# Performance work log

Measured on AMD Instinct MI355X. Metric: run time of the kernel, lower is better.

Reference implementation:

```python
import jax, jax.numpy as jnp
import numpy as np

M = 512          # feature_dim
NH = 8           # num_heads
FFN = 2048       # ffn_hidden_dim
NMOD = 4         # modalities (seq len for attention)
EPS = 1e-5


def setup_inputs() -> dict:
    key = jax.random.key(0)
    ks = jax.random.split(key, 16)
    B, H = 64, 256
    s = 0.02
    return {
        "x_image": jax.random.normal(ks[0], (B, H, M), jnp.float32),
        "x_radar": jax.random.normal(ks[1], (B, H, M), jnp.float32),
        "x_lidar": jax.random.normal(ks[2], (B, H, M), jnp.float32),
        "x_gps":   jax.random.normal(ks[3], (B, H, M), jnp.float32),
        # nn.MultiheadAttention params (torch layout: weight is (out,in))
        "in_proj_w": jax.random.normal(ks[4], (3 * M, M), jnp.float32) * s,
        "in_proj_b": jnp.zeros((3 * M,), jnp.float32),
        "out_proj_w": jax.random.normal(ks[5], (M, M), jnp.float32) * s,
        "out_proj_b": jnp.zeros((M,), jnp.float32),
        "ln1_g": jnp.ones((M,), jnp.float32),
        "ln1_b": jnp.zeros((M,), jnp.float32),
        "w1": jax.random.normal(ks[6], (FFN, M), jnp.float32) * s,
        "b1": jnp.zeros((FFN,), jnp.float32),
        "w2": jax.random.normal(ks[7], (M, FFN), jnp.float32) * s,
        "b2": jnp.zeros((M,), jnp.float32),
        "ln2_g": jnp.ones((M,), jnp.float32),
        "ln2_b": jnpp if False else jnp.zeros((M,), jnp.float32),
    }


def _layernorm(x, g, b):
    mu = jnp.mean(x, axis=-1, keepdims=True)
    var = jnp.mean((x - mu) ** 2, axis=-1, keepdims=True)
    return (x - mu) * jax.lax.rsqrt(var + EPS) * g + b


def _forward(x_image, x_radar, x_lidar, x_gps,
             in_proj_w, in_proj_b, out_proj_w, out_proj_b,
             ln1_g, ln1_b, w1, b1, w2, b2, ln2_g, ln2_b):
    B, H, _ = x_image.shape
    # F: (B*H, NMOD, M) -- fold batch and time; per-t loop is independent
    F = jnp.stack([x_image, x_radar, x_lidar, x_gps], axis=2).reshape(B * H, NMOD, M)
    qkv = F @ in_proj_w.T + in_proj_b              # (N, NMOD, 3M)
    q, k, v = jnp.split(qkv, 3, axis=-1)
    dh = M // NH
    def heads(t):  # (N, NMOD, M) -> (N, NH, NMOD, dh)
        return t.reshape(-1, NMOD, NH, dh).transpose(0, 2, 1, 3)
    qh, kh, vh = heads(q), heads(k), heads(v)
    scores = jnp.einsum("bhsd,bhtd->bhst", qh, kh) / np.sqrt(dh).astype(np.float32)
    attn = jax.nn.softmax(scores, axis=-1)
    o = jnp.einsum("bhst,bhtd->bhsd", attn, vh)
    o = o.transpose(0, 2, 1, 3).reshape(-1, NMOD, M)
    attn_out = o @ out_proj_w.T + out_proj_b
    h1 = _layernorm(F + attn_out, ln1_g, ln1_b)    # (N, NMOD, M)
    agg = h1.sum(axis=1)                            # (N, M)
    ffn = jax.nn.gelu(agg @ w1.T + b1, approximate=False) @ w2.T + b2
    z = _layernorm(agg + ffn, ln2_g, ln2_b)
    return z.reshape(B, H, M)


def reference(x_image, x_radar, x_lidar, x_gps,
              in_proj_w, in_proj_b, out_proj_w, out_proj_b,
              ln1_g, ln1_b, w1, b1, w2, b2, ln2_g, ln2_b):
    return _forward(x_image, x_radar, x_lidar, x_gps,
                    in_proj_w, in_proj_b, out_proj_w, out_proj_b,
                    ln1_g, ln1_b, w1, b1, w2, b2, ln2_g, ln2_b)
```

## Files before the change

kernel.cpp:

```cpp
#include <hip/hip_runtime.h>
#include <hip/hip_bf16.h>


typedef __attribute__((ext_vector_type(8))) short s16x8;
typedef __attribute__((ext_vector_type(4))) float f32x4;

__device__ __forceinline__ unsigned short f2bf(float f) {
  unsigned int u = __float_as_uint(f);
  u += 0x7fffu + ((u >> 16) & 1u);
  return (unsigned short)(u >> 16);
}
__device__ __forceinline__ float bf2f(unsigned short s) {
  return __uint_as_float(((unsigned int)s) << 16);
}
__device__ __forceinline__ f32x4 mfma16(s16x8 a, s16x8 b, f32x4 c) {
  return __builtin_amdgcn_mfma_f32_16x16x32_bf16(a, b, c, 0, 0, 0);
}
__device__ __forceinline__ int swz(int row, int bir) {
  return row * 128 + ((((row) & 7) << 4) ^ bir);
}
__device__ __forceinline__ int vtoff(int r, int c) {
  return r * 1024 + ((c * 2) ^ ((r & 7) << 4));
}

__global__ void pack_kernel(const float* __restrict__ wqkv, const float* __restrict__ wout,
                            const float* __restrict__ w1, const float* __restrict__ w2,
                            const float* __restrict__ x0, const float* __restrict__ x1,
                            const float* __restrict__ x2, const float* __restrict__ x3,
                            unsigned short* __restrict__ o_wqkv, unsigned short* __restrict__ o_wout,
                            unsigned short* __restrict__ o_w1, unsigned short* __restrict__ o_w2,
                            unsigned short* __restrict__ o_x4) {
  const long c0 = 196608, c1 = 262144, c2 = 524288, c3 = 786432, c4 = 9175040;
  for (long v = (long)blockIdx.x * blockDim.x + threadIdx.x; v < c4;
       v += (long)gridDim.x * blockDim.x) {
    const float* src;
    unsigned short* dst;
    if (v < c0) { src = wqkv + v * 4; dst = o_wqkv + v * 4; }
    else if (v < c1) { long u = v - c0; src = wout + u * 4; dst = o_wout + u * 4; }
    else if (v < c2) { long u = v - c1; src = w1 + u * 4; dst = o_w1 + u * 4; }
    else if (v < c3) { long u = v - c2; src = w2 + u * 4; dst = o_w2 + u * 4; }
    else {
      long u = v - c3; long e = u * 4; long r = e >> 9; int i = (int)(e & 511);
      int s = (int)(r & 3); long n = r >> 2;
      const float* xs = (s == 0) ? x0 : (s == 1) ? x1 : (s == 2) ? x2 : x3;
      src = xs + n * 512 + i; dst = o_x4 + e;
    }
    float4 f = *reinterpret_cast<const float4*>(src);
    ushort4 hb;
    hb.x = f2bf(f.x); hb.y = f2bf(f.y); hb.z = f2bf(f.z); hb.w = f2bf(f.w);
    *reinterpret_cast<ushort4*>(dst) = hb;
  }
}

__launch_bounds__(256)
__global__ void qkv_attn_kernel(const unsigned short* __restrict__ x4,
                                const unsigned short* __restrict__ wqkv,
                                const float* __restrict__ in_b,
                                unsigned short* __restrict__ o_out) {
  const int wg = blockIdx.x;
  const int slot = wg >> 3, xcd = wg & 7;
  const int tb = ((slot >> 3) << 3) | xcd;
  const int h = slot & 7;
  const int tid = threadIdx.x, lane = tid & 63, w = tid >> 6;
  const int wm = w >> 1, wn = w & 1;
  const int QS = 200;

  __shared__ __align__(16) unsigned char smem[53248];
  unsigned short* aT = (unsigned short*)smem;
  unsigned short* bT = (unsigned short*)(smem + 16384);
  unsigned short* qkvT = (unsigned short*)smem;
  float* scoresLds = (float*)(smem + 51200);

  f32x4 acc[4][6];
#pragma unroll
  for (int i = 0; i < 4; ++i)
#pragma unroll
    for (int j = 0; j < 6; ++j) acc[i][j] = (f32x4){0.f, 0.f, 0.f, 0.f};

  const long rowBase = (long)tb * 128;

  for (int kk = 0; kk < 8; ++kk) {
    const int k0 = kk * 64;
#pragma unroll
    for (int it = 0; it < 4; ++it) {
      int cid = tid + it * 256, lr = cid >> 3, c8 = cid & 7;
      s16x8 v = *(const s16x8*)(x4 + (rowBase + lr) * 512 + k0 + c8 * 8);
      *(s16x8*)((unsigned char*)aT + swz(lr, c8 * 16)) = v;
    }
#pragma unroll
    for (int it = 0; it < 6; ++it) {
      int cid = tid + it * 256, bc = cid >> 3, c8 = cid & 7;
      int wrow = (bc < 64) ? (h * 64 + bc)
                : (bc < 128) ? (512 + h * 64 + (bc - 64))
                             : (1024 + h * 64 + (bc - 128));
      s16x8 v = *(const s16x8*)(wqkv + (long)wrow * 512 + k0 + c8 * 8);
      *(s16x8*)((unsigned char*)bT + swz(bc, c8 * 16)) = v;
    }
    __syncthreads();
#pragma unroll
    for (int k2 = 0; k2 < 2; ++k2) {
      s16x8 af[4], bfr[6];
      const int bir = k2 * 64 + ((lane >> 4) << 4);
#pragma unroll
      for (int mi = 0; mi < 4; ++mi) {
        int row = wm * 64 + mi * 16 + (lane & 15);
        af[mi] = *(const s16x8*)((unsigned char*)aT + swz(row, bir));
      }
#pragma unroll
      for (int ni = 0; ni < 6; ++ni) {
        int col = wn * 96 + ni * 16 + (lane & 15);
        bfr[ni] = *(const s16x8*)((unsigned char*)bT + swz(col, bir));
      }
#pragma unroll
      for (int mi = 0; mi < 4; ++mi)
#pragma unroll
        for (int ni = 0; ni < 6; ++ni)
          acc[mi][ni] = mfma16(af[mi], bfr[ni], acc[mi][ni]);
    }
    __syncthreads();
  }

#pragma unroll
  for (int mi = 0; mi < 4; ++mi)
#pragma unroll
    for (int ni = 0; ni < 6; ++ni) {
      int col = wn * 96 + ni * 16 + (lane & 15);
      int wrow = (col < 64) ? (h * 64 + col)
                : (col < 128) ? (512 + h * 64 + (col - 64))
                              : (1024 + h * 64 + (col - 128));
      float bias = in_b[wrow];
      int row0 = wm * 64 + mi * 16 + ((lane >> 4) << 2);
#pragma unroll
      for (int r = 0; r < 4; ++r)
        qkvT[(row0 + r) * QS + col] = f2bf(acc[mi][ni][r] + bias);
    }
  __syncthreads();

  const int token = tid >> 3, sub = tid & 7;
  {
    int p0 = sub * 2;
#pragma unroll
    for (int pp = 0; pp < 2; ++pp) {
      int p = p0 + pp, s = p >> 2, t = p & 3;
      const unsigned short* qr = qkvT + (token * 4 + s) * QS;
      const unsigned short* kr = qkvT + (token * 4 + t) * QS + 64;
      float d = 0.f;
#pragma unroll
      for (int c = 0; c < 8; ++c) {
        s16x8 qv = *(const s16x8*)(qr + c * 8);
        s16x8 kv = *(const s16x8*)(kr + c * 8);
#pragma unroll
        for (int i = 0; i < 8; ++i)
          d += bf2f((unsigned short)qv[i]) * bf2f((unsigned short)kv[i]);
      }
      scoresLds[token * 16 + p] = d * 0.125f;
    }
  }
  __syncthreads();
  float attnP[4][4];
#pragma unroll
  for (int s = 0; s < 4; ++s) {
    float m = -1e30f;
#pragma unroll
    for (int t = 0; t < 4; ++t) m = fmaxf(m, scoresLds[token * 16 + s * 4 + t]);
    float sum = 0.f;
#pragma unroll
    for (int t = 0; t < 4; ++t) {
      float e = expf(scoresLds[token * 16 + s * 4 + t] - m);
      attnP[s][t] = e; sum += e;
    }
    float inv = 1.f / sum;
#pragma unroll
    for (int t = 0; t < 4; ++t) attnP[s][t] *= inv;
  }
  float vv[4][8];
#pragma unroll
  for (int t = 0; t < 4; ++t) {
    s16x8 vvec = *(const s16x8*)(qkvT + (token * 4 + t) * QS + 128 + sub * 8);
#pragma unroll
    for (int d = 0; d < 8; ++d) vv[t][d] = bf2f((unsigned short)vvec[d]);
  }
#pragma unroll
  for (int s = 0; s < 4; ++s) {
    long orow = rowBase + token * 4 + s;
    unsigned short* dst = o_out + orow * 512 + h * 64 + sub * 8;
    s16x8 ov;
#pragma unroll
    for (int d = 0; d < 8; ++d) {
      float o = 0.f;
#pragma unroll
      for (int t = 0; t < 4; ++t) o += attnP[s][t] * vv[t][d];
      ov[d] = (short)f2bf(o);
    }
    *(s16x8*)dst = ov;
  }
}

__launch_bounds__(256)
__global__ void outproj_ln1_kernel(const unsigned short* __restrict__ o_in,
                                   const unsigned short* __restrict__ wout,
                                   const float* __restrict__ out_b,
                                   const float* __restrict__ x0, const float* __restrict__ x1,
                                   const float* __restrict__ x2, const float* __restrict__ x3,
                                   const float* __restrict__ ln1_g, const float* __restrict__ ln1_b,
                                   float* __restrict__ agg_f, unsigned short* __restrict__ agg_b) {
  const int tb = blockIdx.x;
  const int tid = threadIdx.x, lane = tid & 63, w = tid >> 6;
  __shared__ __align__(16) unsigned char smem[53504];
  unsigned short* vt = (unsigned short*)smem;
  unsigned short* aT = (unsigned short*)(smem + 32768);
  unsigned short* bT = (unsigned short*)(smem + 36864);
  float* stats = (float*)(smem + 53248);
  const long rowBase = (long)tb * 32;
  const float* xs[4] = {x0, x1, x2, x3};

  for (int ns = 0; ns < 4; ++ns) {
    f32x4 acc[2][2];
#pragma unroll
    for (int i = 0; i < 2; ++i)
#pragma unroll
      for (int j = 0; j < 2; ++j) acc[i][j] = (f32x4){0.f, 0.f, 0.f, 0.f};
    for (int kk = 0; kk < 8; ++kk) {
      const int k0 = kk * 64;
      {
        int lr = tid >> 3, c8 = tid & 7;
        s16x8 v = *(const s16x8*)(o_in + (rowBase + lr) * 512 + k0 + c8 * 8);
        *(s16x8*)((unsigned char*)aT + swz(lr, c8 * 16)) = v;
      }
#pragma unroll
      for (int it = 0; it < 4; ++it) {
        int cid = tid + it * 256, bc = cid >> 3, c8 = cid & 7;
        s16x8 v = *(const s16x8*)(wout + (long)(ns * 128 + bc) * 512 + k0 + c8 * 8);
        *(s16x8*)((unsigned char*)bT + swz(bc, c8 * 16)) = v;
      }
      __syncthreads();
#pragma unroll
      for (int k2 = 0; k2 < 2; ++k2) {
        s16x8 af[2], bfr[2];
        const int bir = k2 * 64 + ((lane >> 4) << 4);
#pragma unroll
        for (int mi = 0; mi < 2; ++mi) {
          int row = mi * 16 + (lane & 15);
          af[mi] = *(const s16x8*)((unsigned char*)aT + swz(row, bir));
        }
#pragma unroll
        for (int ni = 0; ni < 2; ++ni) {
          int col = w * 32 + ni * 16 + (lane & 15);
          bfr[ni] = *(const s16x8*)((unsigned char*)bT + swz(col, bir));
        }
#pragma unroll
        for (int mi = 0; mi < 2; ++mi)
#pragma unroll
          for (int ni = 0; ni < 2; ++ni)
            acc[mi][ni] = mfma16(af[mi], bfr[ni], acc[mi][ni]);
      }
      __syncthreads();
    }
#pragma unroll
    for (int mi = 0; mi < 2; ++mi)
#pragma unroll
      for (int ni = 0; ni < 2; ++ni) {
        int gcol = ns * 128 + w * 32 + ni * 16 + (lane & 15);
        float bias = out_b[gcol];
        int row0 = mi * 16 + ((lane >> 4) << 2);
#pragma unroll
        for (int r = 0; r < 4; ++r) {
          int rr = row0 + r;
          long grow = rowBase + rr;
          int s = (int)(grow & 3); long n = grow >> 2;
          float F = xs[s][n * 512 + gcol];
          *(unsigned short*)((unsigned char*)vt + vtoff(rr, gcol)) =
              f2bf(acc[mi][ni][r] + bias + F);
        }
      }
  }
  __syncthreads();
  {
    int wv = tid >> 6, ln = tid & 63;
    for (int i = 0; i < 8; ++i) {
      int r = wv * 8 + i;
      s16x8 v8 = *(const s16x8*)((unsigned char*)vt + vtoff(r, ln * 8));
      float sum = 0.f, sq = 0.f;
#pragma unroll
      for (int d = 0; d < 8; ++d) {
        float v = bf2f((unsigned short)v8[d]);
        sum += v; sq += v * v;
      }
#pragma unroll
      for (int off = 1; off < 64; off <<= 1) {
        sum += __shfl_xor(sum, off); sq += __shfl_xor(sq, off);
      }
      if (ln == 0) {
        float mu = sum * (1.f / 512.f);
        float var = sq * (1.f / 512.f) - mu * mu;
        stats[r * 2] = mu;
        stats[r * 2 + 1] = rsqrtf(var + 1e-5f);
      }
    }
  }
  __syncthreads();
  for (int it = 0; it < 2; ++it) {
    int ci = tid + it * 256;
    int tok = ci >> 6, c0 = (ci & 63) * 8;
    long gtok = (long)tb * 8 + tok;
    float a[8] = {0.f, 0.f, 0.f, 0.f, 0.f, 0.f, 0.f, 0.f};
#pragma unroll
    for (int s = 0; s < 4; ++s) {
      int r = tok * 4 + s;
      s16x8 v8 = *(const s16x8*)((unsigned char*)vt + vtoff(r, c0));
      float mu = stats[r * 2], is = stats[r * 2 + 1];
#pragma unroll
      for (int d = 0; d < 8; ++d) a[d] += (bf2f((unsigned short)v8[d]) - mu) * is;
    }
    float4 g0 = *(const float4*)(ln1_g + c0);
    float4 g1 = *(const float4*)(ln1_g + c0 + 4);
    float4 b0 = *(const float4*)(ln1_b + c0);
    float4 b1 = *(const float4*)(ln1_b + c0 + 4);
    float ov[8];
    ov[0] = g0.x * a[0] + 4.f * b0.x; ov[1] = g0.y * a[1] + 4.f * b0.y;
    ov[2] = g0.z * a[2] + 4.f * b0.z; ov[3] = g0.w * a[3] + 4.f * b0.w;
    ov[4] = g1.x * a[4] + 4.f * b1.x; ov[5] = g1.y * a[5] + 4.f * b1.y;
    ov[6] = g1.z * a[6] + 4.f * b1.z; ov[7] = g1.w * a[7] + 4.f * b1.w;
    *(float4*)(agg_f + gtok * 512 + c0) = (float4){ov[0], ov[1], ov[2], ov[3]};
    *(float4*)(agg_f + gtok * 512 + c0 + 4) = (float4){ov[4], ov[5], ov[6], ov[7]};
    s16x8 ab;
#pragma unroll
    for (int d = 0; d < 8; ++d) ab[d] = (short)f2bf(ov[d]);
    *(s16x8*)(agg_b + gtok * 512 + c0) = ab;
  }
}

__launch_bounds__(256)
__global__ void ffn1_kernel(const unsigned short* __restrict__ aggb,
                            const unsigned short* __restrict__ w1b,
                            const float* __restrict__ b1,
                            unsigned short* __restrict__ hidden) {
  const int wg = blockIdx.x;
  const int slot = wg >> 3, xcd = wg & 7;
  const int by = ((slot >> 4) << 3) | xcd;
  const int bx = slot & 15;
  const int tid = threadIdx.x, lane = tid & 63, w = tid >> 6;
  const int wm = w >> 1, wn = w & 1;
  __shared__ __align__(16) unsigned char smem[32768];
  unsigned short* aT = (unsigned short*)smem;
  unsigned short* bT = (unsigned short*)(smem + 16384);
  f32x4 acc[4][4];
#pragma unroll
  for (int i = 0; i < 4; ++i)
#pragma unroll
    for (int j = 0; j < 4; ++j) acc[i][j] = (f32x4){0.f, 0.f, 0.f, 0.f};
  const long rowBase = (long)by * 128;
  const long colBase = (long)bx * 128;
  for (int kk = 0; kk < 8; ++kk) {
    const int k0 = kk * 64;
#pragma unroll
    for (int it = 0; it < 4; ++it) {
      int cid = tid + it * 256, lr = cid >> 3, c8 = cid & 7;
      s16x8 v = *(const s16x8*)(aggb + (rowBase + lr) * 512 + k0 + c8 * 8);
      *(s16x8*)((unsigned char*)aT + swz(lr, c8 * 16)) = v;
    }
#pragma unroll
    for (int it = 0; it < 4; ++it) {
      int cid = tid + it * 256, bc = cid >> 3, c8 = cid & 7;
      s16x8 v = *(const s16x8*)(w1b + (colBase + bc) * 512 + k0 + c8 * 8);
      *(s16x8*)((unsigned char*)bT + swz(bc, c8 * 16)) = v;
    }
    __syncthreads();
#pragma unroll
    for (int k2 = 0; k2 < 2; ++k2) {
      s16x8 af[4], bfr[4];
      const int bir = k2 * 64 + ((lane >> 4) << 4);
#pragma unroll
      for (int mi = 0; mi < 4; ++mi) {
        int row = wm * 64 + mi * 16 + (lane & 15);
        af[mi] = *(const s16x8*)((unsigned char*)aT + swz(row, bir));
      }
#pragma unroll
      for (int ni = 0; ni < 4; ++ni) {
        int col = wn * 64 + ni * 16 + (lane & 15);
        bfr[ni] = *(const s16x8*)((unsigned char*)bT + swz(col, bir));
      }
#pragma unroll
      for (int mi = 0; mi < 4; ++mi)
#pragma unroll
        for (int ni = 0; ni < 4; ++ni)
          acc[mi][ni] = mfma16(af[mi], bfr[ni], acc[mi][ni]);
    }
    __syncthreads();
  }
#pragma unroll
  for (int mi = 0; mi < 4; ++mi)
#pragma unroll
    for (int ni = 0; ni < 4; ++ni) {
      long gcol = colBase + wn * 64 + ni * 16 + (lane & 15);
      float bias = b1[gcol];
      int row0 = wm * 64 + mi * 16 + ((lane >> 4) << 2);
#pragma unroll
      for (int r = 0; r < 4; ++r) {
        float x = acc[mi][ni][r] + bias;
        float g = 0.5f * x * (1.f + erff(x * 0.70710678118f));
        hidden[(rowBase + row0 + r) * 2048 + gcol] = f2bf(g);
      }
    }
}

__launch_bounds__(256)
__global__ void ffn2_ln2_kernel(const unsigned short* __restrict__ hidden,
                                const unsigned short* __restrict__ w2b,
                                const float* __restrict__ b2,
                                const float* __restrict__ agg_f,
                                const float* __restrict__ ln2_g,
                                const float* __restrict__ ln2_b,
                                float* __restrict__ out) {
  const int tb = blockIdx.x;
  const int tid = threadIdx.x, lane = tid & 63, w = tid >> 6;
  __shared__ __align__(16) unsigned char smem[53504];
  unsigned short* vt = (unsigned short*)smem;
  unsigned short* aT = (unsigned short*)(smem + 32768);
  unsigned short* bT = (unsigned short*)(smem + 36864);
  float* stats = (float*)(smem + 53248);
  const long rowBase = (long)tb * 32;

  for (int ns = 0; ns < 4; ++ns) {
    f32x4 acc[2][2];
#pragma unroll
    for (int i = 0; i < 2; ++i)
#pragma unroll
      for (int j = 0; j < 2; ++j) acc[i][j] = (f32x4){0.f, 0.f, 0.f, 0.f};
    for (int kk = 0; kk < 32; ++kk) {
      const int k0 = kk * 64;
      {
        int lr = tid >> 3, c8 = tid & 7;
        s16x8 v = *(const s16x8*)(hidden + (rowBase + lr) * 2048 + k0 + c8 * 8);
        *(s16x8*)((unsigned char*)aT + swz(lr, c8 * 16)) = v;
      }
#pragma unroll
      for (int it = 0; it < 4; ++it) {
        int cid = tid + it * 256, bc = cid >> 3, c8 = cid & 7;
        s16x8 v = *(const s16x8*)(w2b + (long)(ns * 128 + bc) * 2048 + k0 + c8 * 8);
        *(s16x8*)((unsigned char*)bT + swz(bc, c8 * 16)) = v;
      }
      __syncthreads();
#pragma unroll
      for (int k2 = 0; k2 < 2; ++k2) {
        s16x8 af[2], bfr[2];
        const int bir = k2 * 64 + ((lane >> 4) << 4);
#pragma unroll
        for (int mi = 0; mi < 2; ++mi) {
          int row = mi * 16 + (lane & 15);
          af[mi] = *(const s16x8*)((unsigned char*)aT + swz(row, bir));
        }
#pragma unroll
        for (int ni = 0; ni < 2; ++ni) {
          int col = w * 32 + ni * 16 + (lane & 15);
          bfr[ni] = *(const s16x8*)((unsigned char*)bT + swz(col, bir));
        }
#pragma unroll
        for (int mi = 0; mi < 2; ++mi)
#pragma unroll
          for (int ni = 0; ni < 2; ++ni)
            acc[mi][ni] = mfma16(af[mi], bfr[ni], acc[mi][ni]);
      }
      __syncthreads();
    }
#pragma unroll
    for (int mi = 0; mi < 2; ++mi)
#pragma unroll
      for (int ni = 0; ni < 2; ++ni) {
        int gcol = ns * 128 + w * 32 + ni * 16 + (lane & 15);
        float bias = b2[gcol];
        int row0 = mi * 16 + ((lane >> 4) << 2);
#pragma unroll
        for (int r = 0; r < 4; ++r) {
          int rr = row0 + r;
          float ag = agg_f[(rowBase + rr) * 512 + gcol];
          *(unsigned short*)((unsigned char*)vt + vtoff(rr, gcol)) =
              f2bf(acc[mi][ni][r] + bias + ag);
        }
      }
  }
  __syncthreads();
  {
    int wv = tid >> 6, ln = tid & 63;
    for (int i = 0; i < 8; ++i) {
      int r = wv * 8 + i;
      s16x8 v8 = *(const s16x8*)((unsigned char*)vt + vtoff(r, ln * 8));
      float sum = 0.f, sq = 0.f;
#pragma unroll
      for (int d = 0; d < 8; ++d) {
        float v = bf2f((unsigned short)v8[d]);
        sum += v; sq += v * v;
      }
#pragma unroll
      for (int off = 1; off < 64; off <<= 1) {
        sum += __shfl_xor(sum, off); sq += __shfl_xor(sq, off);
      }
      if (ln == 0) {
        float mu = sum * (1.f / 512.f);
        float var = sq * (1.f / 512.f) - mu * mu;
        stats[r * 2] = mu;
        stats[r * 2 + 1] = rsqrtf(var + 1e-5f);
      }
    }
  }
  __syncthreads();
  for (int it = 0; it < 8; ++it) {
    int ci = tid + it * 256;
    int r = ci >> 6, c0 = (ci & 63) * 8;
    s16x8 v8 = *(const s16x8*)((unsigned char*)vt + vtoff(r, c0));
    float mu = stats[r * 2], is = stats[r * 2 + 1];
    float4 g0 = *(const float4*)(ln2_g + c0);
    float4 g1 = *(const float4*)(ln2_g + c0 + 4);
    float4 b0 = *(const float4*)(ln2_b + c0);
    float4 b1 = *(const float4*)(ln2_b + c0 + 4);
    float vv[8];
#pragma unroll
    for (int d = 0; d < 8; ++d) vv[d] = (bf2f((unsigned short)v8[d]) - mu) * is;
    float* dst = out + (rowBase + r) * 512 + c0;
    *(float4*)dst = (float4){vv[0] * g0.x + b0.x, vv[1] * g0.y + b0.y,
                             vv[2] * g0.z + b0.z, vv[3] * g0.w + b0.w};
    *(float4*)(dst + 4) = (float4){vv[4] * g1.x + b1.x, vv[5] * g1.y + b1.y,
                                   vv[6] * g1.z + b1.z, vv[7] * g1.w + b1.w};
  }
}

extern "C" void kernel_launch(void* const* d_in, const int* in_sizes, int n_in,
                              void* d_out, int out_size, void* d_ws, size_t ws_size,
                              hipStream_t stream) {
  (void)in_sizes; (void)n_in; (void)out_size;
  const float* x0 = (const float*)d_in[0];
  const float* x1 = (const float*)d_in[1];
  const float* x2 = (const float*)d_in[2];
  const float* x3 = (const float*)d_in[3];
  const float* in_w = (const float*)d_in[4];
  const float* in_b = (const float*)d_in[5];
  const float* out_w = (const float*)d_in[6];
  const float* out_b = (const float*)d_in[7];
  const float* ln1_g = (const float*)d_in[8];
  const float* ln1_b = (const float*)d_in[9];
  const float* w1 = (const float*)d_in[10];
  const float* b1 = (const float*)d_in[11];
  const float* w2 = (const float*)d_in[12];
  const float* b2 = (const float*)d_in[13];
  const float* ln2_g = (const float*)d_in[14];
  const float* ln2_b = (const float*)d_in[15];
  float* out = (float*)d_out;

  unsigned char* ws = (unsigned char*)d_ws;
  if (ws_size < 190840832u) return;
  unsigned short* wqkv_b = (unsigned short*)(ws + 0);
  unsigned short* wout_b = (unsigned short*)(ws + 1572864);
  unsigned short* w1_b = (unsigned short*)(ws + 2097152);
  unsigned short* w2_b = (unsigned short*)(ws + 4194304);
  unsigned short* x4 = (unsigned short*)(ws + 6291456);
  unsigned short* o_buf = (unsigned short*)(ws + 73400320);
  float* agg_f = (float*)(ws + 140509184);
  unsigned short* agg_b = (unsigned short*)(ws + 174063616);
  unsigned short* hidden = o_buf;

  pack_kernel<<<2048, 256, 0, stream>>>(in_w, out_w, w1, w2, x0, x1, x2, x3,
                                        wqkv_b, wout_b, w1_b, w2_b, x4);
  qkv_attn_kernel<<<4096, 256, 0, stream>>>(x4, wqkv_b, in_b, o_buf);
  outproj_ln1_kernel<<<2048, 256, 0, stream>>>(o_buf, wout_b, out_b, x0, x1, x2, x3,
                                               ln1_g, ln1_b, agg_f, agg_b);
  ffn1_kernel<<<2048, 256, 0, stream>>>(agg_b, w1_b, b1, hidden);
  ffn2_ln2_kernel<<<512, 256, 0, stream>>>(hidden, w2_b, b2, agg_f, ln2_g, ln2_b, out);
}
```

Baseline: 490.5 us.

## Use direct global-to-LDS loads in GEMMs and MFMA-based attention core

All GEMM tile loads now use global_load_lds, so data goes straight from global memory into swizzled shared memory with no register round-trip. The swizzle is pre-applied to the source address so the existing fragment reads stay valid. In the QKV kernel, the scalar per-token attention (dot products, softmax via shared scores, PV in registers) is replaced by MFMA QK^T over 16-row tiles. It uses a masked block-diagonal probability matrix, an MFMA PV product against a transposed V in LDS, and a staged coalesced output store. This adds LDS usage and extra barriers, and spends MFMA work on masked zero blocks.

```diff
diff --git a/kernel.cpp b/kernel.cpp
--- a/kernel.cpp
+++ b/kernel.cpp
@@ -19,8 +19,22 @@
 __device__ __forceinline__ int swz(int row, int bir) {
   return row * 128 + ((((row) & 7) << 4) ^ bir);
 }
+__device__ __forceinline__ int qkswz(int row, int c) {
+  return row * 128 + ((((c >> 3) ^ (row & 7)) << 4)) + (c & 7) * 2;
+}
+__device__ __forceinline__ int vtswz(int d, int row) {
+  return d * 256 + ((((row >> 3) ^ (d & 7)) << 4)) + (row & 7) * 2;
+}
+__device__ __forceinline__ int pwswz(int row, int c) {
+  return row * 64 + ((((c >> 3) ^ (row & 3)) << 4)) + (c & 7) * 2;
+}
 __device__ __forceinline__ int vtoff(int r, int c) {
   return r * 1024 + ((c * 2) ^ ((r & 7) << 4));
+}
+__device__ __forceinline__ void gl_lds16(const void* g, void* l) {
+  __builtin_amdgcn_global_load_lds(
+      (const __attribute__((address_space(1))) unsigned int*)g,
+      (__attribute__((address_space(3))) unsigned int*)l, 16, 0, 0);
 }
 
 __global__ void pack_kernel(const float* __restrict__ wqkv, const float* __restrict__ wout,
@@ -63,13 +77,15 @@
   const int h = slot & 7;
   const int tid = threadIdx.x, lane = tid & 63, w = tid >> 6;
   const int wm = w >> 1, wn = w & 1;
-  const int QS = 200;
-
-  __shared__ __align__(16) unsigned char smem[53248];
+
+  __shared__ __align__(16) unsigned char smem[57344];
   unsigned short* aT = (unsigned short*)smem;
   unsigned short* bT = (unsigned short*)(smem + 16384);
-  unsigned short* qkvT = (unsigned short*)smem;
-  float* scoresLds = (float*)(smem + 51200);
+  unsigned short* Qs = (unsigned short*)smem;
+  unsigned short* Ks = (unsigned short*)(smem + 16384);
+  unsigned short* Vt = (unsigned short*)(smem + 32768);
+  unsigned short* Pw = (unsigned short*)(smem + 49152);
+  unsigned short* outT = (unsigned short*)smem;
 
   f32x4 acc[4][6];
 #pragma unroll
@@ -78,23 +94,23 @@
     for (int j = 0; j < 6; ++j) acc[i][j] = (f32x4){0.f, 0.f, 0.f, 0.f};
 
   const long rowBase = (long)tb * 128;
+  const int loff = ((lane >> 3) * 512) + (((lane & 7) ^ (lane >> 3)) * 8);
 
   for (int kk = 0; kk < 8; ++kk) {
     const int k0 = kk * 64;
 #pragma unroll
     for (int it = 0; it < 4; ++it) {
-      int cid = tid + it * 256, lr = cid >> 3, c8 = cid & 7;
-      s16x8 v = *(const s16x8*)(x4 + (rowBase + lr) * 512 + k0 + c8 * 8);
-      *(s16x8*)((unsigned char*)aT + swz(lr, c8 * 16)) = v;
+      int c = w * 4 + it;
+      gl_lds16(x4 + (rowBase + c * 8) * 512 + k0 + loff, aT + c * 512);
     }
 #pragma unroll
     for (int it = 0; it < 6; ++it) {
-      int cid = tid + it * 256, bc = cid >> 3, c8 = cid & 7;
-      int wrow = (bc < 64) ? (h * 64 + bc)
-                : (bc < 128) ? (512 + h * 64 + (bc - 64))
-                             : (1024 + h * 64 + (bc - 128));
-      s16x8 v = *(const s16x8*)(wqkv + (long)wrow * 512 + k0 + c8 * 8);
-      *(s16x8*)((unsigned char*)bT + swz(bc, c8 * 16)) = v;
+      int c = w * 6 + it;
+      int bc0 = c * 8;
+      int wb = (bc0 < 64) ? (h * 64 + bc0)
+             : (bc0 < 128) ? (512 + h * 64 + (bc0 - 64))
+                           : (1024 + h * 64 + (bc0 - 128));
+      gl_lds16(wqkv + (long)wb * 512 + k0 + loff, bT + c * 512);
     }
     __syncthreads();
 #pragma unroll
@@ -125,74 +141,108 @@
 #pragma unroll
     for (int ni = 0; ni < 6; ++ni) {
       int col = wn * 96 + ni * 16 + (lane & 15);
-      int wrow = (col < 64) ? (h * 64 + col)
-                : (col < 128) ? (512 + h * 64 + (col - 64))
-                              : (1024 + h * 64 + (col - 128));
-      float bias = in_b[wrow];
+      int wb = (col < 64) ? (h * 64 + col)
+             : (col < 128) ? (512 + h * 64 + (col - 64))
+                           : (1024 + h * 64 + (col - 128));
+      float bias = in_b[wb];
       int row0 = wm * 64 + mi * 16 + ((lane >> 4) << 2);
 #pragma unroll
+      for (int r = 0; r < 4; ++r) {
+        int row = row0 + r;
+        unsigned short hv = f2bf(acc[mi][ni][r] + bias);
+        if (col < 64)
+          *(unsigned short*)((unsigned char*)Qs + qkswz(row, col)) = hv;
+        else if (col < 128)
+          *(unsigned short*)((unsigned char*)Ks + qkswz(row, col - 64)) = hv;
+        else
+          *(unsigned short*)((unsigned char*)Vt + vtswz(col - 128, row)) = hv;
+      }
+    }
+  __syncthreads();
+
+  f32x4 sacc[2];
+#pragma unroll
+  for (int i2 = 0; i2 < 2; ++i2) {
+    int ti = w * 2 + i2;
+    int qrow = ti * 16 + (lane & 15);
+    int bir = (lane >> 4) << 4;
+    s16x8 qa0 = *(const s16x8*)((unsigned char*)Qs + swz(qrow, bir));
+    s16x8 qa1 = *(const s16x8*)((unsigned char*)Qs + swz(qrow, 64 + bir));
+    s16x8 ka0 = *(const s16x8*)((unsigned char*)Ks + swz(qrow, bir));
+    s16x8 ka1 = *(const s16x8*)((unsigned char*)Ks + swz(qrow, 64 + bir));
+    f32x4 s = (f32x4){0.f, 0.f, 0.f, 0.f};
+    s = mfma16(qa0, ka0, s);
+    s = mfma16(qa1, ka1, s);
+    sacc[i2] = s;
+  }
+  {
+    s16x8 z = (s16x8){0, 0, 0, 0, 0, 0, 0, 0};
+    ((s16x8*)Pw)[tid] = z;
+    ((s16x8*)Pw)[tid + 256] = z;
+  }
+  __syncthreads();
+
+  const bool rel = ((lane & 15) >> 2) == (lane >> 4);
+#pragma unroll
+  for (int i2 = 0; i2 < 2; ++i2) {
+    int ti = w * 2 + i2;
+#pragma unroll
+    for (int r = 0; r < 4; ++r) {
+      float sc = sacc[i2][r] * 0.125f;
+      float m = fmaxf(sc, __shfl_xor(sc, 1));
+      m = fmaxf(m, __shfl_xor(m, 2));
+      float e = __expf(sc - m);
+      float su = e + __shfl_xor(e, 1);
+      su = su + __shfl_xor(su, 2);
+      float p = e / su;
+      if (rel) {
+        int row = ti * 16 + ((lane >> 4) << 2) + r;
+        int cl = (((row >> 2) & 7) << 2) + (lane & 3);
+        *(unsigned short*)((unsigned char*)Pw + pwswz(row, cl)) = f2bf(p);
+      }
+    }
+  }
+  __syncthreads();
+
+  f32x4 pv[2][4];
+#pragma unroll
+  for (int i2 = 0; i2 < 2; ++i2)
+#pragma unroll
+    for (int n = 0; n < 4; ++n) pv[i2][n] = (f32x4){0.f, 0.f, 0.f, 0.f};
+#pragma unroll
+  for (int i2 = 0; i2 < 2; ++i2) {
+    int ti = w * 2 + i2;
+    int arow = ti * 16 + (lane & 15);
+    s16x8 pa = *(const s16x8*)((unsigned char*)Pw + arow * 64 +
+                               ((((lane >> 4) ^ (arow & 3)) << 4)));
+#pragma unroll
+    for (int n = 0; n < 4; ++n) {
+      int d = n * 16 + (lane & 15);
+      int gran = ((ti >> 1) << 2) + (lane >> 4);
+      s16x8 vb = *(const s16x8*)((unsigned char*)Vt + d * 256 +
+                                 (((gran ^ (d & 7)) << 4)));
+      pv[i2][n] = mfma16(pa, vb, pv[i2][n]);
+    }
+  }
+#pragma unroll
+  for (int i2 = 0; i2 < 2; ++i2) {
+    int ti = w * 2 + i2;
+#pragma unroll
+    for (int n = 0; n < 4; ++n) {
+      int d = n * 16 + (lane & 15);
+      int row0 = ti * 16 + ((lane >> 4) << 2);
+#pragma unroll
       for (int r = 0; r < 4; ++r)
-        qkvT[(row0 + r) * QS + col] = f2bf(acc[mi][ni][r] + bias);
-    }
-  __syncthreads();
-
-  const int token = tid >> 3, sub = tid & 7;
-  {
-    int p0 = sub * 2;
-#pragma unroll
-    for (int pp = 0; pp < 2; ++pp) {
-      int p = p0 + pp, s = p >> 2, t = p & 3;
-      const unsigned short* qr = qkvT + (token * 4 + s) * QS;
-      const unsigned short* kr = qkvT + (token * 4 + t) * QS + 64;
-      float d = 0.f;
-#pragma unroll
-      for (int c = 0; c < 8; ++c) {
-        s16x8 qv = *(const s16x8*)(qr + c * 8);
-        s16x8 kv = *(const s16x8*)(kr + c * 8);
-#pragma unroll
-        for (int i = 0; i < 8; ++i)
-          d += bf2f((unsigned short)qv[i]) * bf2f((unsigned short)kv[i]);
-      }
-      scoresLds[token * 16 + p] = d * 0.125f;
-    }
-  }
-  __syncthreads();
-  float attnP[4][4];
-#pragma unroll
-  for (int s = 0; s < 4; ++s) {
-    float m = -1e30f;
-#pragma unroll
-    for (int t = 0; t < 4; ++t) m = fmaxf(m, scoresLds[token * 16 + s * 4 + t]);
-    float sum = 0.f;
-#pragma unroll
-    for (int t = 0; t < 4; ++t) {
-      float e = expf(scoresLds[token * 16 + s * 4 + t] - m);
-      attnP[s][t] = e; sum += e;
-    }
-    float inv = 1.f / sum;
-#pragma unroll
-    for (int t = 0; t < 4; ++t) attnP[s][t] *= inv;
-  }
-  float vv[4][8];
-#pragma unroll
-  for (int t = 0; t < 4; ++t) {
-    s16x8 vvec = *(const s16x8*)(qkvT + (token * 4 + t) * QS + 128 + sub * 8);
-#pragma unroll
-    for (int d = 0; d < 8; ++d) vv[t][d] = bf2f((unsigned short)vvec[d]);
-  }
-#pragma unroll
-  for (int s = 0; s < 4; ++s) {
-    long orow = rowBase + token * 4 + s;
-    unsigned short* dst = o_out + orow * 512 + h * 64 + sub * 8;
-    s16x8 ov;
-#pragma unroll
-    for (int d = 0; d < 8; ++d) {
-      float o = 0.f;
-#pragma unroll
-      for (int t = 0; t < 4; ++t) o += attnP[s][t] * vv[t][d];
-      ov[d] = (short)f2bf(o);
-    }
-    *(s16x8*)dst = ov;
+        outT[(row0 + r) * 72 + d] = f2bf(pv[i2][n][r]);
+    }
+  }
+  __syncthreads();
+#pragma unroll
+  for (int j = 0; j < 4; ++j) {
+    int c = j * 256 + tid;
+    int row = c >> 3, ch = c & 7;
+    s16x8 v = *(const s16x8*)(outT + row * 72 + ch * 8);
+    *(s16x8*)(o_out + (rowBase + row) * 512 + h * 64 + ch * 8) = v;
   }
 }
 
@@ -213,6 +263,7 @@
   float* stats = (float*)(smem + 53248);
   const long rowBase = (long)tb * 32;
   const float* xs[4] = {x0, x1, x2, x3};
+  const int loff = ((lane >> 3) * 512) + (((lane & 7) ^ (lane >> 3)) * 8);
 
   for (int ns = 0; ns < 4; ++ns) {
     f32x4 acc[2][2];
@@ -222,16 +273,11 @@
       for (int j = 0; j < 2; ++j) acc[i][j] = (f32x4){0.f, 0.f, 0.f, 0.f};
     for (int kk = 0; kk < 8; ++kk) {
       const int k0 = kk * 64;
-      {
-        int lr = tid >> 3, c8 = tid & 7;
-        s16x8 v = *(const s16x8*)(o_in + (rowBase + lr) * 512 + k0 + c8 * 8);
-        *(s16x8*)((unsigned char*)aT + swz(lr, c8 * 16)) = v;
-      }
+      gl_lds16(o_in + (rowBase + w * 8) * 512 + k0 + loff, aT + w * 512);
 #pragma unroll
       for (int it = 0; it < 4; ++it) {
-        int cid = tid + it * 256, bc = cid >> 3, c8 = cid & 7;
-        s16x8 v = *(const s16x8*)(wout + (long)(ns * 128 + bc) * 512 + k0 + c8 * 8);
-        *(s16x8*)((unsigned char*)bT + swz(bc, c8 * 16)) = v;
+        int c = w * 4 + it;
+        gl_lds16(wout + (long)(ns * 128 + c * 8) * 512 + k0 + loff, bT + c * 512);
       }
       __syncthreads();
 #pragma unroll
@@ -351,19 +397,18 @@
     for (int j = 0; j < 4; ++j) acc[i][j] = (f32x4){0.f, 0.f, 0.f, 0.f};
   const long rowBase = (long)by * 128;
   const long colBase = (long)bx * 128;
+  const int loff = ((lane >> 3) * 512) + (((lane & 7) ^ (lane >> 3)) * 8);
   for (int kk = 0; kk < 8; ++kk) {
     const int k0 = kk * 64;
 #pragma unroll
     for (int it = 0; it < 4; ++it) {
-      int cid = tid + it * 256, lr = cid >> 3, c8 = cid & 7;
-      s16x8 v = *(const s16x8*)(aggb + (rowBase + lr) * 512 + k0 + c8 * 8);
-      *(s16x8*)((unsigned char*)aT + swz(lr, c8 * 16)) = v;
+      int c = w * 4 + it;
+      gl_lds16(aggb + (rowBase + c * 8) * 512 + k0 + loff, aT + c * 512);
     }
 #pragma unroll
     for (int it = 0; it < 4; ++it) {
-      int cid = tid + it * 256, bc = cid >> 3, c8 = cid & 7;
-      s16x8 v = *(const s16x8*)(w1b + (colBase + bc) * 512 + k0 + c8 * 8);
-      *(s16x8*)((unsigned char*)bT + swz(bc, c8 * 16)) = v;
+      int c = w * 4 + it;
+      gl_lds16(w1b + (colBase + c * 8) * 512 + k0 + loff, bT + c * 512);
     }
     __syncthreads();
 #pragma unroll
@@ -420,6 +465,7 @@
   unsigned short* bT = (unsigned short*)(smem + 36864);
   float* stats = (float*)(smem + 53248);
   const long rowBase = (long)tb * 32;
+  const int loff4 = ((lane >> 3) * 2048) + (((lane & 7) ^ (lane >> 3)) * 8);
 
   for (int ns = 0; ns < 4; ++ns) {
     f32x4 acc[2][2];
@@ -429,16 +475,11 @@
       for (int j = 0; j < 2; ++j) acc[i][j] = (f32x4){0.f, 0.f, 0.f, 0.f};
     for (int kk = 0; kk < 32; ++kk) {
       const int k0 = kk * 64;
-      {
-        int lr = tid >> 3, c8 = tid & 7;
-        s16x8 v = *(const s16x8*)(hidden + (rowBase + lr) * 2048 + k0 + c8 * 8);
-        *(s16x8*)((unsigned char*)aT + swz(lr, c8 * 16)) = v;
-      }
+      gl_lds16(hidden + (rowBase + w * 8) * 2048 + k0 + loff4, aT + w * 512);
 #pragma unroll
       for (int it = 0; it < 4; ++it) {
-        int cid = tid + it * 256, bc = cid >> 3, c8 = cid & 7;
-        s16x8 v = *(const s16x8*)(w2b + (long)(ns * 128 + bc) * 2048 + k0 + c8 * 8);
-        *(s16x8*)((unsigned char*)bT + swz(bc, c8 * 16)) = v;
+        int c = w * 4 + it;
+        gl_lds16(w2b + (long)(ns * 128 + c * 8) * 2048 + k0 + loff4, bT + c * 512);
       }
       __syncthreads();
 #pragma unroll
```

Result: slower. 690.0 us (+40.7%).
